# Kernel optimization log

Measured on AMD Instinct MI355X. Metric: run time of the kernel, lower is better.

## Reference

```python
import jax, jax.numpy as jnp
from jax import lax
import numpy as np

SIGMA = 1.0
E_THETA = 0.1
E_ALPHA = 1.0
THETA = 0.1
T_NCE = 0.07
EPS = 1e-7


def setup_inputs() -> dict:
    key = jax.random.key(0)
    ks = jax.random.split(key, 11)
    B, NC, K, C, TLEN = 64, 20, 150, 2048, 750
    return {
        "video_scores": jax.random.uniform(ks[0], (B, NC), jnp.float32, EPS, 1.0 - EPS),
        "label": jax.random.uniform(ks[1], (B, NC), jnp.float32, 0.1, 1.0),
        "HA": jax.random.normal(ks[2], (B, K, C), jnp.float32),
        "EA": jax.random.normal(ks[3], (B, K, C), jnp.float32),
        "HB": jax.random.normal(ks[4], (B, K, C), jnp.float32),
        "EB": jax.random.normal(ks[5], (B, K, C), jnp.float32),
        "re_s_scores": jax.random.uniform(ks[6], (2, B, TLEN), jnp.float32),
        "re_d_scores": jax.random.uniform(ks[7], (2, B, TLEN), jnp.float32),
        "actioness": jax.random.uniform(ks[8], (B, TLEN), jnp.float32),
        "actioness_2": jax.random.uniform(ks[9], (B, TLEN), jnp.float32),
        "attention_scores": jax.random.uniform(ks[10], (B, 2 * K, 1), jnp.float32),
    }


def _nce(q, k, neg, att):
    # q,k: [B,C]; neg: [B,K,C]; att: [B,K]
    qn = q / jnp.linalg.norm(q, axis=1, keepdims=True)
    kn = k / jnp.linalg.norm(k, axis=1, keepdims=True)
    negp = jnp.swapaxes(neg, 1, 2)                       # [B,C,K]
    negn = negp / jnp.linalg.norm(negp, axis=1, keepdims=True)
    l_pos = jnp.einsum('nc,nc->n', qn, kn)[:, None]      # [B,1]
    l_neg = att * jnp.einsum('nc,nck->nk', qn, negn)     # [B,K]
    logits = jnp.concatenate([l_pos, l_neg], axis=1) / T_NCE
    # CrossEntropy with target class 0 for every row
    return jnp.mean(-jax.nn.log_softmax(logits, axis=1)[:, 0])


def _pad11(x):
    # matches torch: [:, :6]=first col, [:, -6:]=last col, [:, 6:-5]=data (overwrites idx 755)
    return jnp.concatenate(
        [jnp.repeat(x[:, :1], 6, axis=1), x, jnp.repeat(x[:, -1:], 5, axis=1)], axis=1)


def reference(video_scores, label, HA, EA, HB, EB, re_s_scores, re_d_scores,
              actioness, actioness_2, attention_scores):
    # ---- ActionLoss (BCE with normalized label) ----
    lab = label / jnp.sum(label, axis=1, keepdims=True)
    vs = jnp.clip(video_scores, EPS, 1.0 - EPS)
    loss_cls = -jnp.mean(lab * jnp.log(vs) + (1.0 - lab) * jnp.log1p(-vs))

    # ---- SniCoLoss_v5 ----
    loss_snico = (_nce(HA.mean(1), EA.mean(1), EB, attention_scores[:, :150, 0])
                  + _nce(HB.mean(1), EB.mean(1), EA, attention_scores[:, 150:300, 0]))

    # ---- RelationLoss (sum of per-tensor means / len == mean of stacked) ----
    loss_rel = jnp.mean((1.0 - re_s_scores) ** 2) + jnp.mean(re_d_scores ** 2)

    # ---- ActELoss_v2 (vectorized sliding-window weighted L1, fuses 750x11 loop) ----
    a0 = lax.stop_gradient(actioness)        # actioness.detach() in TotalLoss
    a3 = _pad11(actioness_2)                 # [B,761]
    a4 = lax.stop_gradient(_pad11(a0))       # [B,761]
    idx = jnp.arange(750)[:, None] + jnp.arange(11)      # [750,11]
    a4w = a4[:, idx]                                     # [B,750,11]
    a3w = lax.stop_gradient(a3)[:, idx]                  # [B,750,11]
    # w_ij = exp(-||a0[:,i]-a4[:,i+j]||_2^2 / (2 sigma^2)), norm over batch dim
    w = jnp.exp(-jnp.sum((a0[:, :, None] - a4w) ** 2, axis=0) / (2.0 * SIGMA * SIGMA))  # [750,11]
    absm = jnp.mean(jnp.abs(actioness_2[:, :, None] - a3w), axis=0)                     # [750,11]
    loss_act = jnp.sum(w * absm)
    loss_act = loss_act + jnp.mean(E_THETA * jnp.sum((a0 - actioness_2) ** 2, axis=1))
    loss_act = loss_act * E_ALPHA

    loss_total = loss_cls + 0.01 * loss_snico + loss_act + THETA * loss_rel
    return (loss_total, loss_cls, loss_snico, loss_act, loss_rel)
```

## Files before the change

### kernel.cpp

```cpp
#include <hip/hip_runtime.h>
#include <hip/hip_bf16.h>
#include <math.h>

#define T_NCE 0.07f
#define EPSF 1e-7f

#define WS_MEANS 32
#define MEANS_N (4 * 64 * 2048)
#define WS_DOTS (WS_MEANS + MEANS_N)
#define WS_NSQ  (WS_DOTS + 2 * 64 * 150)

__device__ __forceinline__ float bf2f(unsigned short h) {
    unsigned int u = ((unsigned int)h) << 16;
    float f;
    __builtin_memcpy(&f, &u, 4);
    return f;
}

__device__ __forceinline__ float ldf(const void* p, int i, int bf) {
    if (bf) return bf2f(((const unsigned short*)p)[i]);
    return ((const float*)p)[i];
}

struct F8 { float v[8]; };

__device__ __forceinline__ F8 ld8(const void* p, int i, int bf) {
    F8 r;
    if (bf) {
        uint4 u = *((const uint4*)((const unsigned short*)p + i));
        const unsigned short* hs = (const unsigned short*)&u;
#pragma unroll
        for (int k = 0; k < 8; k++) r.v[k] = bf2f(hs[k]);
    } else {
        const float4* q = (const float4*)((const float*)p + i);
        float4 a = q[0], b = q[1];
        r.v[0] = a.x; r.v[1] = a.y; r.v[2] = a.z; r.v[3] = a.w;
        r.v[4] = b.x; r.v[5] = b.y; r.v[6] = b.z; r.v[7] = b.w;
    }
    return r;
}

__device__ __forceinline__ float block_reduce256(float v, float* sbuf) {
    int t = threadIdx.x;
    sbuf[t] = v;
    __syncthreads();
    for (int s = 128; s > 0; s >>= 1) {
        if (t < s) sbuf[t] += sbuf[t + s];
        __syncthreads();
    }
    float r = sbuf[0];
    __syncthreads();
    return r;
}

__device__ __forceinline__ float block_reduce_max256(float v, float* sbuf) {
    int t = threadIdx.x;
    sbuf[t] = v;
    __syncthreads();
    for (int s = 128; s > 0; s >>= 1) {
        if (t < s) sbuf[t] = fmaxf(sbuf[t], sbuf[t + s]);
        __syncthreads();
    }
    float r = sbuf[0];
    __syncthreads();
    return r;
}

__global__ void k_zero(const void* video_scores, float* ws) {
    int gid = blockIdx.x * 256 + threadIdx.x;
    float4* m4 = (float4*)(ws + WS_MEANS);
    if (gid < MEANS_N / 4) m4[gid] = make_float4(0.f, 0.f, 0.f, 0.f);
    if (gid == 0) {
        const unsigned short* u = (const unsigned short*)video_scores;
        int cnt = 0;
        for (int i = 0; i < 64; i++) {
            unsigned short h = u[2 * i];
            int e = (h >> 7) & 0xFF;
            int sgn = (h >> 15) & 1;
            if (!sgn && e >= 90 && e <= 126) cnt++;
        }
        ((int*)ws)[0] = (cnt >= 56) ? 1 : 0;
        ws[8] = 0.f; ws[9] = 0.f; ws[10] = 0.f; ws[11] = 0.f;
    }
}

__global__ void k_means(const void* HA, const void* EA, const void* HB, const void* EB,
                        float* ws) {
    int bf = ((const int*)ws)[0];
    int bi = blockIdx.x;
    int chunk = bi % 5;
    int b = (bi / 5) & 63;
    int arr = bi / 320;
    const void* src = (arr == 0) ? HA : (arr == 1) ? EA : (arr == 2) ? HB : EB;
    int c0 = threadIdx.x * 8;
    float acc[8];
#pragma unroll
    for (int k = 0; k < 8; k++) acc[k] = 0.f;
    int j0 = chunk * 30;
    for (int j = j0; j < j0 + 30; j++) {
        F8 v = ld8(src, (b * 150 + j) * 2048 + c0, bf);
#pragma unroll
        for (int k = 0; k < 8; k++) acc[k] += v.v[k];
    }
    float* dst = ws + WS_MEANS + (arr * 64 + b) * 2048 + c0;
#pragma unroll
    for (int k = 0; k < 8; k++) atomicAdd(dst + k, acc[k]);
}

__global__ void k_dots(const void* EA, const void* EB, float* ws) {
    int bf = ((const int*)ws)[0];
    int bi = blockIdx.x;
    int which = bi / 960;
    int rem = bi % 960;
    int b = rem / 15;
    int chunk = rem % 15;
    int lane = threadIdx.x & 63;
    int wid = threadIdx.x >> 6;

    const float* qb = ws + WS_MEANS + ((which == 0 ? 0 : 2) * 64 + b) * 2048;
    float qreg[32];
#pragma unroll
    for (int it = 0; it < 4; it++) {
        const float4* p = (const float4*)(qb + it * 512 + lane * 8);
        float4 a = p[0], c = p[1];
        qreg[it * 8 + 0] = a.x; qreg[it * 8 + 1] = a.y;
        qreg[it * 8 + 2] = a.z; qreg[it * 8 + 3] = a.w;
        qreg[it * 8 + 4] = c.x; qreg[it * 8 + 5] = c.y;
        qreg[it * 8 + 6] = c.z; qreg[it * 8 + 7] = c.w;
    }

    const void* neg = (which == 0) ? EB : EA;
    for (int j = chunk * 10 + wid; j < chunk * 10 + 10; j += 4) {
        int base = (b * 150 + j) * 2048;
        float dot = 0.f, nsq = 0.f;
#pragma unroll
        for (int it = 0; it < 4; it++) {
            int off = it * 512 + lane * 8;
            F8 v = ld8(neg, base + off, bf);
#pragma unroll
            for (int k = 0; k < 8; k++) {
                float x = v.v[k];
                dot += x * qreg[it * 8 + k];
                nsq += x * x;
            }
        }
        for (int s = 32; s > 0; s >>= 1) {
            dot += __shfl_down(dot, s);
            nsq += __shfl_down(nsq, s);
        }
        if (lane == 0) {
            ws[WS_DOTS + (which * 64 + b) * 150 + j] = dot;
            ws[WS_NSQ + (which * 64 + b) * 150 + j] = nsq;
        }
    }
}

__global__ void k_small(const void* vs, const void* label,
                        const void* res, const void* red,
                        const void* a0, const void* a2, float* ws) {
    int bf = ((const int*)ws)[0];
    __shared__ float sbuf[256];
    __shared__ float rowsum[64];
    __shared__ float sa0[64 * 40];
    __shared__ float sa2[64 * 40];
    int t = threadIdx.x;
    int bi = blockIdx.x;

    if (bi == 0) {
        if (t < 64) {
            float s = 0.f;
            for (int c = 0; c < 20; c++) s += ldf(label, t * 20 + c, bf);
            rowsum[t] = s;
        }
        __syncthreads();
        float local = 0.f;
        for (int i = t; i < 1280; i += 256) {
            int b = i / 20;
            float lab = ldf(label, i, bf) / rowsum[b];
            float v = ldf(vs, i, bf);
            v = fminf(fmaxf(v, EPSF), 1.f - EPSF);
            local += lab * logf(v) + (1.f - lab) * log1pf(-v);
        }
        float s = block_reduce256(local, sbuf);
        if (t == 0) ws[8] = -s / 1280.f;
    } else if (bi <= 32) {
        int base = (bi - 1) * 256 + t;
        int stride = 32 * 256;
        float lrel = 0.f;
        for (int i = base; i < 96000; i += stride) {
            float sv = ldf(res, i, bf);
            float dv = ldf(red, i, bf);
            lrel += (1.f - sv) * (1.f - sv) + dv * dv;
        }
        float s = block_reduce256(lrel, sbuf);
        if (t == 0) atomicAdd(&ws[9], s * (1.f / 96000.f));
        float lact = 0.f;
        for (int i = base; i < 48000; i += stride) {
            float x = ldf(a0, i, bf) - ldf(a2, i, bf);
            lact += x * x;
        }
        s = block_reduce256(lact, sbuf);
        if (t == 0) atomicAdd(&ws[10], s * (0.1f / 64.f));
    } else {
        int abi = bi - 33;
        int B0 = abi * 256;
        int B1 = min(B0 + 255, 8249);
        int tmin = B0 / 11, tmax = B1 / 11;
        int lo = max(0, tmin - 6);
        int hi = min(749, tmax + 5);
        int ncol = hi - lo + 1;
        int total = 64 * ncol;
        for (int i = t; i < total; i += 256) {
            int b = i / ncol;
            int col = i % ncol;
            sa0[i] = ldf(a0, b * 750 + lo + col, bf);
            sa2[i] = ldf(a2, b * 750 + lo + col, bf);
        }
        __syncthreads();
        int id = B0 + t;
        float val = 0.f;
        if (id < 8250) {
            int tt = id / 11;
            int d = id % 11;
            int c = min(max(tt + d - 6, 0), 749);
            int ct = tt - lo, cc = c - lo;
            float wsum = 0.f, asum = 0.f;
            for (int b = 0; b < 64; b++) {
                float x = sa0[b * ncol + ct];
                float y = sa0[b * ncol + cc];
                wsum += (x - y) * (x - y);
                float p = sa2[b * ncol + ct];
                float q = sa2[b * ncol + cc];
                asum += fabsf(p - q);
            }
            val = __expf(-0.5f * wsum) * (asum * (1.f / 64.f));
        }
        float s = block_reduce256(val, sbuf);
        if (t == 0) atomicAdd(&ws[10], s);
    }
}

__global__ void k_nce(const void* att, float* ws) {
    int bf = ((const int*)ws)[0];
    __shared__ float sbuf[256];
    int t = threadIdx.x;
    int w = blockIdx.x >> 6;
    int b = blockIdx.x & 63;
    const float* qv = ws + WS_MEANS + ((w == 0 ? 0 : 2) * 64 + b) * 2048;
    const float* kv = ws + WS_MEANS + ((w == 0 ? 1 : 3) * 64 + b) * 2048;
    float p0 = 0.f, p1 = 0.f, p2 = 0.f;
    for (int c = t; c < 2048; c += 256) {
        float qa = qv[c], ka = kv[c];
        p0 += qa * qa; p1 += ka * ka; p2 += qa * ka;
    }
    float nq = block_reduce256(p0, sbuf);
    float nk = block_reduce256(p1, sbuf);
    float dd = block_reduce256(p2, sbuf);
    float invq = rsqrtf(nq);
    float lpos = dd * invq * rsqrtf(nk) * (1.f / T_NCE);
    float lg = -INFINITY;
    if (t < 150) {
        float raw = ws[WS_DOTS + (w * 64 + b) * 150 + t];
        float nn = ws[WS_NSQ + (w * 64 + b) * 150 + t];
        float a = ldf(att, b * 300 + w * 150 + t, bf);
        lg = a * raw * invq * rsqrtf(nn) * (1.f / T_NCE);
    }
    float m = block_reduce_max256(lg, sbuf);
    m = fmaxf(m, lpos);
    float ex = (t < 150) ? expf(lg - m) : 0.f;
    float ssum = block_reduce256(ex, sbuf) + expf(lpos - m);
    if (t == 0) {
        float loss = (m + logf(ssum)) - lpos;
        atomicAdd(&ws[11], loss * (1.f / 64.f));
    }
}

__global__ void k_out(float* ws, void* out) {
    if (threadIdx.x == 0) {
        int bf = ((const int*)ws)[0];
        float cls = ws[8], rel = ws[9], act = ws[10], snico = ws[11];
        float total = cls + 0.01f * snico + act + 0.1f * rel;
        if (bf) {
            __hip_bfloat16* o = (__hip_bfloat16*)out;
            o[0] = __float2bfloat16(total);
            o[1] = __float2bfloat16(cls);
            o[2] = __float2bfloat16(snico);
            o[3] = __float2bfloat16(act);
            o[4] = __float2bfloat16(rel);
        } else {
            float* o = (float*)out;
            o[0] = total; o[1] = cls; o[2] = snico; o[3] = act; o[4] = rel;
        }
    }
}

extern "C" void kernel_launch(void* const* d_in, const int* in_sizes, int n_in,
                              void* d_out, int out_size, void* d_ws, size_t ws_size,
                              hipStream_t stream) {
    const void* video_scores = d_in[0];
    const void* label = d_in[1];
    const void* HA = d_in[2];
    const void* EA = d_in[3];
    const void* HB = d_in[4];
    const void* EB = d_in[5];
    const void* re_s = d_in[6];
    const void* re_d = d_in[7];
    const void* actioness = d_in[8];
    const void* actioness_2 = d_in[9];
    const void* att = d_in[10];
    float* ws = (float*)d_ws;

    k_zero<<<512, 256, 0, stream>>>(video_scores, ws);
    k_means<<<1280, 256, 0, stream>>>(HA, EA, HB, EB, ws);
    k_dots<<<1920, 256, 0, stream>>>(EA, EB, ws);
    k_small<<<66, 256, 0, stream>>>(video_scores, label, re_s, re_d,
                                    actioness, actioness_2, ws);
    k_nce<<<128, 256, 0, stream>>>(att, ws);
    k_out<<<1, 1, 0, stream>>>(ws, d_out);
}
```

Before: 374.3 us.

## Replace atomic mean accumulation with per-block LDS reduction and drop zeroing pass

The means kernel now assigns each block a 512-column stripe of one batch row and splits the 150 rows across 8 waves, then reduces the partial sums in shared memory and writes them directly. Because the writes are no longer atomic, the workspace no longer needs zeroing, so the zero kernel shrinks to a single-thread format check. This removes global atomic traffic and a memset pass over 2 MB. The cost is fewer, larger blocks with a shared-memory reduction and a barrier.

```diff
diff --git a/kernel.cpp b/kernel.cpp
--- a/kernel.cpp
+++ b/kernel.cpp
@@ -67,10 +67,7 @@
 }
 
 __global__ void k_zero(const void* video_scores, float* ws) {
-    int gid = blockIdx.x * 256 + threadIdx.x;
-    float4* m4 = (float4*)(ws + WS_MEANS);
-    if (gid < MEANS_N / 4) m4[gid] = make_float4(0.f, 0.f, 0.f, 0.f);
-    if (gid == 0) {
+    if (threadIdx.x == 0) {
         const unsigned short* u = (const unsigned short*)video_scores;
         int cnt = 0;
         for (int i = 0; i < 64; i++) {
@@ -87,24 +84,47 @@
 __global__ void k_means(const void* HA, const void* EA, const void* HB, const void* EB,
                         float* ws) {
     int bf = ((const int*)ws)[0];
+    __shared__ float part[8][512];
     int bi = blockIdx.x;
-    int chunk = bi % 5;
-    int b = (bi / 5) & 63;
-    int arr = bi / 320;
+    int stripe = bi & 3;
+    int b = (bi >> 2) & 63;
+    int arr = bi >> 8;
     const void* src = (arr == 0) ? HA : (arr == 1) ? EA : (arr == 2) ? HB : EB;
-    int c0 = threadIdx.x * 8;
+    int t = threadIdx.x;
+    int lane = t & 63;
+    int wid = t >> 6;
+    int c0 = stripe * 512 + lane * 8;
+    int ib = b * 150 * 2048 + c0;
+
     float acc[8];
 #pragma unroll
     for (int k = 0; k < 8; k++) acc[k] = 0.f;
-    int j0 = chunk * 30;
-    for (int j = j0; j < j0 + 30; j++) {
-        F8 v = ld8(src, (b * 150 + j) * 2048 + c0, bf);
+
+    int j = wid;
+    for (; j + 24 < 150; j += 32) {
+        F8 v0 = ld8(src, ib + (j + 0) * 2048, bf);
+        F8 v1 = ld8(src, ib + (j + 8) * 2048, bf);
+        F8 v2 = ld8(src, ib + (j + 16) * 2048, bf);
+        F8 v3 = ld8(src, ib + (j + 24) * 2048, bf);
+#pragma unroll
+        for (int k = 0; k < 8; k++)
+            acc[k] += (v0.v[k] + v1.v[k]) + (v2.v[k] + v3.v[k]);
+    }
+    for (; j < 150; j += 8) {
+        F8 v = ld8(src, ib + j * 2048, bf);
 #pragma unroll
         for (int k = 0; k < 8; k++) acc[k] += v.v[k];
     }
-    float* dst = ws + WS_MEANS + (arr * 64 + b) * 2048 + c0;
-#pragma unroll
-    for (int k = 0; k < 8; k++) atomicAdd(dst + k, acc[k]);
+
+#pragma unroll
+    for (int k = 0; k < 8; k++) part[wid][lane * 8 + k] = acc[k];
+    __syncthreads();
+
+    float* dst = ws + WS_MEANS + (arr * 64 + b) * 2048 + stripe * 512;
+    float s = part[0][t & 511];
+#pragma unroll
+    for (int w = 1; w < 8; w++) s += part[w][t & 511];
+    dst[t & 511] = s;
 }
 
 __global__ void k_dots(const void* EA, const void* EB, float* ws) {
@@ -310,8 +330,8 @@
     const void* att = d_in[10];
     float* ws = (float*)d_ws;
 
-    k_zero<<<512, 256, 0, stream>>>(video_scores, ws);
-    k_means<<<1280, 256, 0, stream>>>(HA, EA, HB, EB, ws);
+    k_zero<<<1, 64, 0, stream>>>(video_scores, ws);
+    k_means<<<1024, 512, 0, stream>>>(HA, EA, HB, EB, ws);
     k_dots<<<1920, 256, 0, stream>>>(EA, EB, ws);
     k_small<<<66, 256, 0, stream>>>(video_scores, label, re_s, re_d,
                                     actioness, actioness_2, ws);
```

Measured after the change: 346.3 us. 7.5% less time.

## Replace atomic means with per-batch shared-memory reduction and batch row loads

Applied to the files above, without the earlier changes.

k_means now uses one 1024-thread block per (array,batch). Four row groups each accumulate every fourth row and are summed in shared memory, then written directly, which removes the zeroing pass and the global atomics. k_zero shrinks to a single thread that does dtype detection. k_means and the bf16 path of k_dots issue several wide loads up front before accumulating to raise memory-level parallelism. The catch is fewer, larger blocks (256) and more registers per thread, which may lower occupancy on a bandwidth-bound read of about 300MB.

```diff
diff --git a/kernel.cpp b/kernel.cpp
--- a/kernel.cpp
+++ b/kernel.cpp
@@ -67,10 +67,7 @@
 }
 
 __global__ void k_zero(const void* video_scores, float* ws) {
-    int gid = blockIdx.x * 256 + threadIdx.x;
-    float4* m4 = (float4*)(ws + WS_MEANS);
-    if (gid < MEANS_N / 4) m4[gid] = make_float4(0.f, 0.f, 0.f, 0.f);
-    if (gid == 0) {
+    if (threadIdx.x == 0) {
         const unsigned short* u = (const unsigned short*)video_scores;
         int cnt = 0;
         for (int i = 0; i < 64; i++) {
@@ -84,27 +81,94 @@
     }
 }
 
-__global__ void k_means(const void* HA, const void* EA, const void* HB, const void* EB,
-                        float* ws) {
+__global__ __launch_bounds__(1024) void k_means(const void* HA, const void* EA,
+                                                const void* HB, const void* EB,
+                                                float* ws) {
     int bf = ((const int*)ws)[0];
+    __shared__ float part[4][2048];
     int bi = blockIdx.x;
-    int chunk = bi % 5;
-    int b = (bi / 5) & 63;
-    int arr = bi / 320;
+    int b = bi & 63;
+    int arr = bi >> 6;
     const void* src = (arr == 0) ? HA : (arr == 1) ? EA : (arr == 2) ? HB : EB;
-    int c0 = threadIdx.x * 8;
+    int t = threadIdx.x;
+    int ct = t & 255;
+    int g = t >> 8;
+    int base = b * 150 * 2048 + ct * 8;
+
     float acc[8];
 #pragma unroll
-    for (int k = 0; k < 8; k++) acc[k] = 0.f;
-    int j0 = chunk * 30;
-    for (int j = j0; j < j0 + 30; j++) {
-        F8 v = ld8(src, (b * 150 + j) * 2048 + c0, bf);
-#pragma unroll
-        for (int k = 0; k < 8; k++) acc[k] += v.v[k];
-    }
-    float* dst = ws + WS_MEANS + (arr * 64 + b) * 2048 + c0;
-#pragma unroll
-    for (int k = 0; k < 8; k++) atomicAdd(dst + k, acc[k]);
+    for (int e = 0; e < 8; e++) acc[e] = 0.f;
+
+    if (bf) {
+        const unsigned short* sp = (const unsigned short*)src;
+        int j = g;
+        for (int batch = 0; batch < 5; batch++) {
+            uint4 r[8];
+#pragma unroll
+            for (int k = 0; k < 8; k++) {
+                int jj = j + 4 * k;
+                if (jj < 150) r[k] = *(const uint4*)(sp + base + jj * 2048);
+            }
+#pragma unroll
+            for (int k = 0; k < 8; k++) {
+                int jj = j + 4 * k;
+                if (jj < 150) {
+                    const unsigned short* hs = (const unsigned short*)&r[k];
+#pragma unroll
+                    for (int e = 0; e < 8; e++) acc[e] += bf2f(hs[e]);
+                }
+            }
+            j += 32;
+        }
+    } else {
+        const float* fp = (const float*)src;
+        int j = g;
+        for (int batch = 0; batch < 10; batch++) {
+            float4 r[4][2];
+#pragma unroll
+            for (int k = 0; k < 4; k++) {
+                int jj = j + 4 * k;
+                if (jj < 150) {
+                    const float4* p = (const float4*)(fp + base + jj * 2048);
+                    r[k][0] = p[0];
+                    r[k][1] = p[1];
+                }
+            }
+#pragma unroll
+            for (int k = 0; k < 4; k++) {
+                int jj = j + 4 * k;
+                if (jj < 150) {
+                    acc[0] += r[k][0].x; acc[1] += r[k][0].y;
+                    acc[2] += r[k][0].z; acc[3] += r[k][0].w;
+                    acc[4] += r[k][1].x; acc[5] += r[k][1].y;
+                    acc[6] += r[k][1].z; acc[7] += r[k][1].w;
+                }
+            }
+            j += 16;
+        }
+    }
+
+#pragma unroll
+    for (int e = 0; e < 8; e++) part[g][ct * 8 + e] = acc[e];
+    __syncthreads();
+
+    float* dst = ws + WS_MEANS + (arr * 64 + b) * 2048;
+    for (int c = t; c < 2048; c += 1024)
+        dst[c] = part[0][c] + part[1][c] + part[2][c] + part[3][c];
+}
+
+__device__ __forceinline__ void dotrow_bf(const uint4* r, const float* qreg,
+                                          float& dot, float& nsq) {
+#pragma unroll
+    for (int it = 0; it < 4; it++) {
+        const unsigned short* hs = (const unsigned short*)&r[it];
+#pragma unroll
+        for (int k = 0; k < 8; k++) {
+            float x = bf2f(hs[k]);
+            dot += x * qreg[it * 8 + k];
+            nsq += x * x;
+        }
+    }
 }
 
 __global__ void k_dots(const void* EA, const void* EB, float* ws) {
@@ -130,27 +194,70 @@
     }
 
     const void* neg = (which == 0) ? EB : EA;
-    for (int j = chunk * 10 + wid; j < chunk * 10 + 10; j += 4) {
-        int base = (b * 150 + j) * 2048;
-        float dot = 0.f, nsq = 0.f;
-#pragma unroll
-        for (int it = 0; it < 4; it++) {
-            int off = it * 512 + lane * 8;
-            F8 v = ld8(neg, base + off, bf);
-#pragma unroll
-            for (int k = 0; k < 8; k++) {
-                float x = v.v[k];
-                dot += x * qreg[it * 8 + k];
-                nsq += x * x;
-            }
-        }
+    int e0 = chunk * 10;
+    int outb = WS_DOTS + (which * 64 + b) * 150;
+    int nsqb = WS_NSQ + (which * 64 + b) * 150;
+
+    if (bf) {
+        const unsigned short* np = (const unsigned short*)neg;
+        int jA = e0 + wid;
+        int jB = jA + 4;
+        int jC = jA + 8;
+        uint4 rA[4], rB[4];
+#pragma unroll
+        for (int it = 0; it < 4; it++)
+            rA[it] = *(const uint4*)(np + (b * 150 + jA) * 2048 + it * 512 + lane * 8);
+#pragma unroll
+        for (int it = 0; it < 4; it++)
+            rB[it] = *(const uint4*)(np + (b * 150 + jB) * 2048 + it * 512 + lane * 8);
+        float dA = 0.f, nA = 0.f, dB = 0.f, nB = 0.f;
+        dotrow_bf(rA, qreg, dA, nA);
+        dotrow_bf(rB, qreg, dB, nB);
         for (int s = 32; s > 0; s >>= 1) {
-            dot += __shfl_down(dot, s);
-            nsq += __shfl_down(nsq, s);
+            dA += __shfl_down(dA, s); nA += __shfl_down(nA, s);
+            dB += __shfl_down(dB, s); nB += __shfl_down(nB, s);
         }
         if (lane == 0) {
-            ws[WS_DOTS + (which * 64 + b) * 150 + j] = dot;
-            ws[WS_NSQ + (which * 64 + b) * 150 + j] = nsq;
+            ws[outb + jA] = dA; ws[nsqb + jA] = nA;
+            ws[outb + jB] = dB; ws[nsqb + jB] = nB;
+        }
+        if (jC < e0 + 10) {
+            uint4 rC[4];
+#pragma unroll
+            for (int it = 0; it < 4; it++)
+                rC[it] = *(const uint4*)(np + (b * 150 + jC) * 2048 + it * 512 + lane * 8);
+            float dC = 0.f, nC = 0.f;
+            dotrow_bf(rC, qreg, dC, nC);
+            for (int s = 32; s > 0; s >>= 1) {
+                dC += __shfl_down(dC, s); nC += __shfl_down(nC, s);
+            }
+            if (lane == 0) {
+                ws[outb + jC] = dC; ws[nsqb + jC] = nC;
+            }
+        }
+    } else {
+        for (int j = e0 + wid; j < e0 + 10; j += 4) {
+            int base = (b * 150 + j) * 2048;
+            float dot = 0.f, nsq = 0.f;
+#pragma unroll
+            for (int it = 0; it < 4; it++) {
+                int off = it * 512 + lane * 8;
+                F8 v = ld8(neg, base + off, 0);
+#pragma unroll
+                for (int k = 0; k < 8; k++) {
+                    float x = v.v[k];
+                    dot += x * qreg[it * 8 + k];
+                    nsq += x * x;
+                }
+            }
+            for (int s = 32; s > 0; s >>= 1) {
+                dot += __shfl_down(dot, s);
+                nsq += __shfl_down(nsq, s);
+            }
+            if (lane == 0) {
+                ws[outb + j] = dot;
+                ws[nsqb + j] = nsq;
+            }
         }
     }
 }
@@ -310,8 +417,8 @@
     const void* att = d_in[10];
     float* ws = (float*)d_ws;
 
-    k_zero<<<512, 256, 0, stream>>>(video_scores, ws);
-    k_means<<<1280, 256, 0, stream>>>(HA, EA, HB, EB, ws);
+    k_zero<<<1, 64, 0, stream>>>(video_scores, ws);
+    k_means<<<256, 1024, 0, stream>>>(HA, EA, HB, EB, ws);
     k_dots<<<1920, 256, 0, stream>>>(EA, EB, ws);
     k_small<<<66, 256, 0, stream>>>(video_scores, label, re_s, re_d,
                                     actioness, actioness_2, ws);
```

New measurement: 434.8 us. 16.2% more time.
